# Optimization experiments

Measured on AMD Instinct MI355X. Metric: run time of the kernel, lower is better.

## Reference

```python
import math
import jax, jax.numpy as jnp
import numpy as np

NEG_INF = -jnp.inf


def setup_inputs() -> dict:
    key = jax.random.key(0)
    k1, k2, k3 = jax.random.split(key, 3)
    B, T, D = 2, 2048, 1024
    x = jax.random.normal(k1, (B, T, D), dtype=jnp.float32)
    w_qkv = jax.random.normal(k2, (3 * D, D), dtype=jnp.float32) * (1.0 / math.sqrt(D))
    w_out = jax.random.normal(k3, (D, D), dtype=jnp.float32) * (1.0 / math.sqrt(D))
    return {"x": x, "w_qkv": w_qkv, "w_out": w_out, "n_heads": 16, "k": 8}


def reference(x, w_qkv, w_out, n_heads, k):
    B, T, D = x.shape
    head_dim = D // n_heads
    scale = math.sqrt(head_dim)

    qkv = x @ w_qkv.T                                   # (B,T,3D), torch Linear: x W^T
    q, kk, v = jnp.split(qkv, 3, axis=-1)

    def split_heads(t):
        return t.reshape(B, T, n_heads, head_dim).transpose(0, 2, 1, 3)  # (B,H,T,dh)

    q, kk, v = split_heads(q), split_heads(kk), split_heads(v)

    scores = jnp.einsum("bhqd,bhkd->bhqk", q, kk) / scale  # (B,H,T,T)
    causal = jnp.tril(jnp.ones((T, T), dtype=bool))
    scores = jnp.where(causal, scores, NEG_INF)

    # per-row effective k: min(k, n_valid) with n_valid = row index + 1
    top_vals = jax.lax.top_k(scores, k)[0]                 # (B,H,T,k), sorted desc
    k_eff_idx = jnp.minimum(jnp.arange(1, T + 1), k) - 1   # (T,)
    thresh = jnp.take_along_axis(
        top_vals, k_eff_idx[None, None, :, None], axis=-1  # (B,H,T,1)
    )
    keep = scores >= thresh                                # ties kept, matching torch >=
    scores = jnp.where(keep, scores, NEG_INF)

    attn = jax.nn.softmax(scores, axis=-1)
    attn = jnp.nan_to_num(attn)                            # defensive; rows never all -inf
    out = jnp.einsum("bhqk,bhkd->bhqd", attn, v)
    out = out.transpose(0, 2, 1, 3).reshape(B, T, D)       # merge heads
    return out @ w_out.T
```

## Files before the change

### kernel.cpp

```cpp
#include <hip/hip_runtime.h>
#include <hip/hip_bf16.h>
#include <math.h>
#include <float.h>

#define NUM_B 2
#define SEQ_T 2048
#define DIM_D 1024
#define NH 16
#define DH 64
#define KDIM 1024
#define KSEL 8

#define CAP 32
#define MFMA_MARGIN 0.06f

typedef __attribute__((ext_vector_type(8))) short bf16x8v;
typedef __attribute__((ext_vector_type(4))) float f32x4v;
typedef __attribute__((ext_vector_type(4))) double f64x4v;

__device__ __forceinline__ float bf2f(unsigned int u) {
  union { unsigned int i; float f; } v; v.i = u << 16; return v.f;
}

__device__ __forceinline__ short f2bs(float f) {
  __hip_bfloat16 h = __float2bfloat16(f);
  return *(short*)&h;
}

__device__ __forceinline__ void split8(float4 x0, float4 x1,
                                       unsigned short* __restrict__ hp,
                                       unsigned short* __restrict__ lp) {
  unsigned short h[8], l[8];
  const float xs[8] = {x0.x, x0.y, x0.z, x0.w, x1.x, x1.y, x1.z, x1.w};
#pragma unroll
  for (int j = 0; j < 8; ++j) {
    const short hb = f2bs(xs[j]);
    h[j] = (unsigned short)hb;
    const float hf = bf2f((unsigned int)(unsigned short)hb);
    l[j] = (unsigned short)f2bs(xs[j] - hf);
  }
  *(uint4*)hp = *(const uint4*)h;
  *(uint4*)lp = *(const uint4*)l;
}

__device__ __forceinline__ void split4(float4 x,
                                       unsigned short* __restrict__ hp,
                                       unsigned short* __restrict__ lp) {
  unsigned short h[4], l[4];
  const float xs[4] = {x.x, x.y, x.z, x.w};
#pragma unroll
  for (int j = 0; j < 4; ++j) {
    const short hb = f2bs(xs[j]);
    h[j] = (unsigned short)hb;
    const float hf = bf2f((unsigned int)(unsigned short)hb);
    l[j] = (unsigned short)f2bs(xs[j] - hf);
  }
  *(uint2*)hp = *(const uint2*)h;
  *(uint2*)lp = *(const uint2*)l;
}

__global__ __launch_bounds__(512) void gemm_qk(
    const float* __restrict__ A, const float* __restrict__ Bm,
    float* __restrict__ qbuf, float* __restrict__ kbuf,
    unsigned short* __restrict__ kbf) {
  __shared__ __align__(16) float As[64][36];
  __shared__ __align__(16) float Bs[128][36];
  const int tid = threadIdx.x;
  const int lane = tid & 63;
  const int w = tid >> 6;
  const int row0 = blockIdx.y * 64;
  const int col0 = blockIdx.x * 128;
  const int lrA = tid >> 3;
  const int lkA = (tid & 7) << 2;
  const int lrB = tid >> 2;
  const int lkB = (tid & 3) << 3;
  const float* ap = A + (size_t)(row0 + lrA) * KDIM + lkA;
  const float* bp = Bm + (size_t)(col0 + lrB) * KDIM + lkB;
  const int wr = (w >> 2) << 5;
  const int wc = (w & 3) << 5;
  const int li = lane & 15;
  const int lk4 = lane >> 4;

  int rowof[4], colof[4];
  {
    f64x4v pr = {0.0, 0.0, 0.0, 0.0};
    f64x4v pc = {0.0, 0.0, 0.0, 0.0};
    const double vidx = (double)li;
    pr = __builtin_amdgcn_mfma_f64_16x16x4f64(vidx, 1.0, pr, 0, 0, 0);
    pc = __builtin_amdgcn_mfma_f64_16x16x4f64(1.0, vidx, pc, 0, 0, 0);
#pragma unroll
    for (int vj = 0; vj < 4; ++vj) {
      rowof[vj] = (int)(pr[vj] * 0.25 + 0.5);
      colof[vj] = (int)(pc[vj] * 0.25 + 0.5);
    }
  }

  f64x4v acc[2][2];
#pragma unroll
  for (int m = 0; m < 2; ++m)
#pragma unroll
    for (int n = 0; n < 2; ++n)
      acc[m][n] = (f64x4v){0.0, 0.0, 0.0, 0.0};

  float4 ra = *(const float4*)(ap);
  float4 rb0 = *(const float4*)(bp);
  float4 rb1 = *(const float4*)(bp + 4);
  for (int k0 = 0; k0 < KDIM; k0 += 32) {
    __syncthreads();
    *(float4*)&As[lrA][lkA] = ra;
    *(float4*)&Bs[lrB][lkB] = rb0;
    *(float4*)&Bs[lrB][lkB + 4] = rb1;
    if (k0 + 32 < KDIM) {
      ra = *(const float4*)(ap + k0 + 32);
      rb0 = *(const float4*)(bp + k0 + 32);
      rb1 = *(const float4*)(bp + k0 + 36);
    }
    __syncthreads();
#pragma unroll
    for (int ks = 0; ks < 32; ks += 4) {
      const int kk = ks + lk4;
      const double af0 = (double)As[wr + li][kk];
      const double af1 = (double)As[wr + 16 + li][kk];
      const double bf0 = (double)Bs[wc + li][kk];
      const double bf1 = (double)Bs[wc + 16 + li][kk];
      acc[0][0] = __builtin_amdgcn_mfma_f64_16x16x4f64(af0, bf0, acc[0][0], 0, 0, 0);
      acc[0][1] = __builtin_amdgcn_mfma_f64_16x16x4f64(af0, bf1, acc[0][1], 0, 0, 0);
      acc[1][0] = __builtin_amdgcn_mfma_f64_16x16x4f64(af1, bf0, acc[1][0], 0, 0, 0);
      acc[1][1] = __builtin_amdgcn_mfma_f64_16x16x4f64(af1, bf1, acc[1][1], 0, 0, 0);
    }
  }

  const int bb = row0 >> 11;
  const int t0 = row0 & 2047;
#pragma unroll
  for (int m = 0; m < 2; ++m)
#pragma unroll
    for (int n = 0; n < 2; ++n)
#pragma unroll
      for (int vj = 0; vj < 4; ++vj) {
        const int r = wr + 16 * m + rowof[vj];
        const int gc = col0 + wc + 16 * n + colof[vj];
        const int qi = gc >> 10;
        const int head = (gc & 1023) >> 6;
        const int d = gc & 63;
        const int t = t0 + r;
        const float fv = (float)acc[m][n][vj];
        float* dst = ((qi == 0) ? qbuf : kbuf) +
                     (size_t)(bb * NH + head) * SEQ_T * DH;
        dst[(size_t)t * DH + d] = fv;
        if (qi == 1) {
          unsigned short* kb = kbf + ((size_t)(bb * NH + head) << 17);
          const int key = t & 127;
          const int off =
              (((t >> 7) << 13) | (key << 6) | d) ^ ((key & 7) << 3);
          __hip_bfloat16 hb = __float2bfloat16(fv);
          kb[off] = *(unsigned short*)&hb;
        }
      }
}

__global__ __launch_bounds__(512) void gemm_v(
    const float* __restrict__ A, const float* __restrict__ Bm,
    unsigned short* __restrict__ vbuf) {
  __shared__ __align__(16) unsigned short Ah[64][40];
  __shared__ __align__(16) unsigned short Al[64][40];
  __shared__ __align__(16) unsigned short Bh[128][40];
  __shared__ __align__(16) unsigned short Bl[128][40];
  const int tid = threadIdx.x;
  const int lane = tid & 63;
  const int w = tid >> 6;
  const int row0 = blockIdx.y * 64;
  const int col0v = blockIdx.x * 128;
  const int lrA = tid >> 3;
  const int lkA = (tid & 7) << 2;
  const int lrB = tid >> 2;
  const int lkB = (tid & 3) << 3;
  const float* ap = A + (size_t)(row0 + lrA) * KDIM + lkA;
  const float* bp = Bm + (size_t)(col0v + lrB) * KDIM + lkB;
  const int wr = (w >> 2) << 5;
  const int wc = (w & 3) << 5;
  const int li = lane & 15;
  const int kA = (lane >> 4) << 3;

  f32x4v acc[2][2];
#pragma unroll
  for (int m = 0; m < 2; ++m)
#pragma unroll
    for (int n = 0; n < 2; ++n)
      acc[m][n] = (f32x4v){0.f, 0.f, 0.f, 0.f};

  float4 ra = *(const float4*)(ap);
  float4 rb0 = *(const float4*)(bp);
  float4 rb1 = *(const float4*)(bp + 4);
  for (int k0 = 0; k0 < KDIM; k0 += 32) {
    __syncthreads();
    split4(ra, &Ah[lrA][lkA], &Al[lrA][lkA]);
    split8(rb0, rb1, &Bh[lrB][lkB], &Bl[lrB][lkB]);
    if (k0 + 32 < KDIM) {
      ra = *(const float4*)(ap + k0 + 32);
      rb0 = *(const float4*)(bp + k0 + 32);
      rb1 = *(const float4*)(bp + k0 + 36);
    }
    __syncthreads();
    bf16x8v ah[2], al[2], bh[2], bl[2];
#pragma unroll
    for (int m = 0; m < 2; ++m) {
      ah[m] = *(const bf16x8v*)&Ah[wr + 16 * m + li][kA];
      al[m] = *(const bf16x8v*)&Al[wr + 16 * m + li][kA];
      bh[m] = *(const bf16x8v*)&Bh[wc + 16 * m + li][kA];
      bl[m] = *(const bf16x8v*)&Bl[wc + 16 * m + li][kA];
    }
#pragma unroll
    for (int m = 0; m < 2; ++m)
#pragma unroll
      for (int n = 0; n < 2; ++n) {
        acc[m][n] = __builtin_amdgcn_mfma_f32_16x16x32_bf16(ah[m], bh[n], acc[m][n], 0, 0, 0);
        acc[m][n] = __builtin_amdgcn_mfma_f32_16x16x32_bf16(ah[m], bl[n], acc[m][n], 0, 0, 0);
        acc[m][n] = __builtin_amdgcn_mfma_f32_16x16x32_bf16(al[m], bh[n], acc[m][n], 0, 0, 0);
      }
  }

  const int bb = row0 >> 11;
  const int t0 = row0 & 2047;
  const int r4 = (lane >> 4) << 2;
#pragma unroll
  for (int m = 0; m < 2; ++m)
#pragma unroll
    for (int n = 0; n < 2; ++n)
#pragma unroll
      for (int j = 0; j < 4; ++j) {
        const int t = t0 + wr + 16 * m + r4 + j;
        const int vcol = col0v + wc + 16 * n + li;
        const int head = vcol >> 6;
        const int d = vcol & 63;
        vbuf[(size_t)(bb * NH + head) * SEQ_T * DH + (size_t)t * DH + d] =
            (unsigned short)f2bs(acc[m][n][j]);
      }
}

__global__ __launch_bounds__(512) void attn_topk(
    const float* __restrict__ q, const float* __restrict__ kmat,
    const unsigned short* __restrict__ kbf,
    const unsigned short* __restrict__ v, unsigned short* __restrict__ ctx) {
  __shared__ __align__(16) unsigned short kt[128 * 64];
  __shared__ double cs64[128][CAP];
  __shared__ short ckey[128][CAP];
  __shared__ int ccnt[128];
  __shared__ double rthr[128];
  __shared__ float rmx[128];

  const int tid = threadIdx.x;
  const int lane = tid & 63;
  const int w = tid >> 6;
  const int bh = blockIdx.x & 31;
  const int u = blockIdx.x >> 5;
  const int g = (u < 8) ? u : 23 - u;
  const int t0 = g << 7;
  const size_t kbase = (size_t)bh * SEQ_T * DH;
  const int wrow0 = t0 + (w << 4);
  const int kA = (lane >> 4) << 3;
  const int rbase = wrow0 + ((lane >> 4) << 2);

  bf16x8v qa0, qa1;
  {
    const float* qr = q + kbase + (size_t)(wrow0 + (lane & 15)) * DH;
    const float4 x0 = *(const float4*)(qr + kA);
    const float4 x1 = *(const float4*)(qr + kA + 4);
    const float4 y0 = *(const float4*)(qr + 32 + kA);
    const float4 y1 = *(const float4*)(qr + 32 + kA + 4);
    qa0[0] = f2bs(x0.x); qa0[1] = f2bs(x0.y);
    qa0[2] = f2bs(x0.z); qa0[3] = f2bs(x0.w);
    qa0[4] = f2bs(x1.x); qa0[5] = f2bs(x1.y);
    qa0[6] = f2bs(x1.z); qa0[7] = f2bs(x1.w);
    qa1[0] = f2bs(y0.x); qa1[1] = f2bs(y0.y);
    qa1[2] = f2bs(y0.z); qa1[3] = f2bs(y0.w);
    qa1[4] = f2bs(y1.x); qa1[5] = f2bs(y1.y);
    qa1[6] = f2bs(y1.z); qa1[7] = f2bs(y1.w);
  }

  const uint4* ksrc = (const uint4*)(kbf + ((size_t)bh << 17));
  const int nt = (t0 >> 7) + 1;
  const int wmax = wrow0 + 15;

  float tq[4][8];
#pragma unroll
  for (int j = 0; j < 4; ++j)
#pragma unroll
    for (int m = 0; m < 8; ++m) tq[j][m] = -FLT_MAX;

  for (int T = 0; T < nt; ++T) {
    if (T) __syncthreads();
    {
      const uint4* st = ksrc + (size_t)T * 1024;
      uint4* dv = (uint4*)kt;
#pragma unroll
      for (int i = 0; i < 2; ++i) dv[i * 512 + tid] = st[i * 512 + tid];
    }
    __syncthreads();
    const int glim0 = (wmax - (T << 7)) >> 4;
    const int glim = glim0 > 7 ? 7 : glim0;
    for (int gt = 0; gt <= glim; ++gt) {
      const int kk = (gt << 4) + (lane & 15);
      const int key = (T << 7) + kk;
      const int b0 = ((kk << 7) | (kA << 1)) ^ ((kk & 7) << 4);
      const int b1 = ((kk << 7) | ((32 + kA) << 1)) ^ ((kk & 7) << 4);
      const bf16x8v kb0 = *(const bf16x8v*)((const char*)kt + b0);
      const bf16x8v kb1 = *(const bf16x8v*)((const char*)kt + b1);
      f32x4v acc = {0.f, 0.f, 0.f, 0.f};
      acc = __builtin_amdgcn_mfma_f32_16x16x32_bf16(qa0, kb0, acc, 0, 0, 0);
      acc = __builtin_amdgcn_mfma_f32_16x16x32_bf16(qa1, kb1, acc, 0, 0, 0);
#pragma unroll
      for (int j = 0; j < 4; ++j) {
        float sc = acc[j] * 0.125f;
        sc = (key <= rbase + j) ? sc : -FLT_MAX;
        if (sc > tq[j][7]) {
          float s = sc;
#pragma unroll
          for (int m = 0; m < 8; ++m) {
            const float hi = fmaxf(tq[j][m], s);
            s = fminf(tq[j][m], s);
            tq[j][m] = hi;
          }
        }
      }
    }
  }

#pragma unroll
  for (int j = 0; j < 4; ++j) {
#pragma unroll
    for (int xm = 1; xm < 16; xm <<= 1) {
      float m[8];
#pragma unroll
      for (int i = 0; i < 8; ++i) {
        const float pb = __shfl_xor(tq[j][7 - i], xm);
        m[i] = fmaxf(tq[j][i], pb);
      }
#pragma unroll
      for (int d = 4; d >= 1; d >>= 1)
#pragma unroll
        for (int i = 0; i < 8; ++i)
          if ((i & d) == 0 && (i | d) < 8) {
            const float hi = fmaxf(m[i], m[i | d]);
            const float lo = fminf(m[i], m[i | d]);
            m[i] = hi;
            m[i | d] = lo;
          }
#pragma unroll
      for (int i = 0; i < 8; ++i) tq[j][i] = m[i];
    }
  }
  float thrj[4];
#pragma unroll
  for (int j = 0; j < 4; ++j) {
    const int kf = (rbase + j + 1 < KSEL) ? (rbase + j + 1) : KSEL;
    float th = tq[j][7];
#pragma unroll
    for (int m = 0; m < 8; ++m)
      if (m == kf - 1) th = tq[j][m];
    thrj[j] = th - MFMA_MARGIN;
  }

  if (tid < 128) ccnt[tid] = 0;
  __syncthreads();

  for (int T = 0; T < nt; ++T) {
    if (T) __syncthreads();
    {
      const uint4* st = ksrc + (size_t)T * 1024;
      uint4* dv = (uint4*)kt;
#pragma unroll
      for (int i = 0; i < 2; ++i) dv[i * 512 + tid] = st[i * 512 + tid];
    }
    __syncthreads();
    const int glim0 = (wmax - (T << 7)) >> 4;
    const int glim = glim0 > 7 ? 7 : glim0;
    for (int gt = 0; gt <= glim; ++gt) {
      const int kk = (gt << 4) + (lane & 15);
      const int key = (T << 7) + kk;
      const int b0 = ((kk << 7) | (kA << 1)) ^ ((kk & 7) << 4);
      const int b1 = ((kk << 7) | ((32 + kA) << 1)) ^ ((kk & 7) << 4);
      const bf16x8v kb0 = *(const bf16x8v*)((const char*)kt + b0);
      const bf16x8v kb1 = *(const bf16x8v*)((const char*)kt + b1);
      f32x4v acc = {0.f, 0.f, 0.f, 0.f};
      acc = __builtin_amdgcn_mfma_f32_16x16x32_bf16(qa0, kb0, acc, 0, 0, 0);
      acc = __builtin_amdgcn_mfma_f32_16x16x32_bf16(qa1, kb1, acc, 0, 0, 0);
#pragma unroll
      for (int j = 0; j < 4; ++j) {
        const float sc = acc[j] * 0.125f;
        if (key <= rbase + j && sc >= thrj[j]) {
          const int rl = (w << 4) + ((lane >> 4) << 2) + j;
          const int p = atomicAdd(&ccnt[rl], 1);
          if (p < CAP) ckey[rl][p] = (short)key;
        }
      }
    }
  }

  const int lid = lane & 31;
  for (int rp = 0; rp < 8; ++rp) {
    const int rl = (w << 4) + (rp << 1) + (lane >> 5);
    const int ncc = ccnt[rl] < CAP ? ccnt[rl] : CAP;
    if (lid < ncc) {
      const int key = ckey[rl][lid];
      const float* qr = q + kbase + (size_t)(t0 + rl) * DH;
      const float* kr = kmat + kbase + (size_t)key * DH;
      double s = 0.0;
#pragma unroll
      for (int d4 = 0; d4 < 16; ++d4) {
        const float4 qq = *(const float4*)(qr + (d4 << 2));
        const float4 kq = *(const float4*)(kr + (d4 << 2));
        s = fma((double)qq.x, (double)kq.x, s);
        s = fma((double)qq.y, (double)kq.y, s);
        s = fma((double)qq.z, (double)kq.z, s);
        s = fma((double)qq.w, (double)kq.w, s);
      }
      cs64[rl][lid] = s * 0.125;
    }
  }
  __syncthreads();

  if (lane < 16) {
    const int rl = (w << 4) + lane;
    const int trow = t0 + rl;
    const int ncc = ccnt[rl] < CAP ? ccnt[rl] : CAP;
    double a64[8];
#pragma unroll
    for (int j = 0; j < 8; ++j) a64[j] = -DBL_MAX;
    for (int l = 0; l < ncc; ++l) {
      double sv = cs64[rl][l];
#pragma unroll
      for (int j = 0; j < 8; ++j) {
        const double hi = fmax(a64[j], sv);
        sv = fmin(a64[j], sv);
        a64[j] = hi;
      }
    }
    const int kf = (trow + 1 < KSEL) ? (trow + 1) : KSEL;
    double th = a64[7];
#pragma unroll
    for (int j = 0; j < 8; ++j)
      if (j == kf - 1) th = a64[j];
    rthr[rl] = th;
    rmx[rl] = (float)a64[0];
  }
  __syncthreads();

  for (int rg = 0; rg < 4; ++rg) {
    const int rlb = (w << 4) + (rg << 2);
    float acv[4] = {0.f, 0.f, 0.f, 0.f};
    float Zs[4] = {0.f, 0.f, 0.f, 0.f};
    int ncs[4];
    double ths[4];
    float mxs[4];
#pragma unroll
    for (int j = 0; j < 4; ++j) {
      const int rl = rlb + j;
      ncs[j] = ccnt[rl] < CAP ? ccnt[rl] : CAP;
      ths[j] = rthr[rl];
      mxs[j] = rmx[rl];
    }
    int nmax = ncs[0];
#pragma unroll
    for (int j = 1; j < 4; ++j) nmax = ncs[j] > nmax ? ncs[j] : nmax;
    for (int l = 0; l < nmax; ++l) {
#pragma unroll
      for (int j = 0; j < 4; ++j) {
        const int rl = rlb + j;
        if (l < ncs[j]) {
          const double s = cs64[rl][l];
          const float wgl = (s >= ths[j]) ? expf((float)s - mxs[j]) : 0.f;
          Zs[j] += wgl;
          acv[j] = fmaf(
              wgl,
              bf2f((unsigned int)v[kbase + (size_t)ckey[rl][l] * DH + lane]),
              acv[j]);
        }
      }
    }
#pragma unroll
    for (int j = 0; j < 4; ++j) {
      const int trow = t0 + rlb + j;
      __hip_bfloat16 h = __float2bfloat16(acv[j] / Zs[j]);
      ctx[((size_t)(bh >> 4) * SEQ_T + trow) * DIM_D + (bh & 15) * DH + lane] =
          *(unsigned short*)&h;
    }
  }
}

__global__ __launch_bounds__(512) void gemm_out(
    const unsigned short* __restrict__ A, const float* __restrict__ Bm,
    float* __restrict__ obuf) {
  __shared__ __align__(16) unsigned short Ah[64][40];
  __shared__ __align__(16) unsigned short Bh[128][40];
  __shared__ __align__(16) unsigned short Bl[128][40];
  const int tid = threadIdx.x;
  const int lane = tid & 63;
  const int w = tid >> 6;
  const int row0 = blockIdx.y * 64;
  const int col0 = blockIdx.x * 128;
  const int lrA = tid >> 3;
  const int lkA = (tid & 7) << 2;
  const int lrB = tid >> 2;
  const int lkB = (tid & 3) << 3;
  const unsigned short* ap = A + (size_t)(row0 + lrA) * KDIM + lkA;
  const float* bp = Bm + (size_t)(col0 + lrB) * KDIM + lkB;
  const int wr = (w >> 2) << 5;
  const int wc = (w & 3) << 5;
  const int li = lane & 15;
  const int kA = (lane >> 4) << 3;

  f32x4v acc[2][2];
#pragma unroll
  for (int m = 0; m < 2; ++m)
#pragma unroll
    for (int n = 0; n < 2; ++n)
      acc[m][n] = (f32x4v){0.f, 0.f, 0.f, 0.f};

  uint2 ua = *(const uint2*)(ap);
  float4 rb0 = *(const float4*)(bp);
  float4 rb1 = *(const float4*)(bp + 4);
  for (int k0 = 0; k0 < KDIM; k0 += 32) {
    __syncthreads();
    *(uint2*)&Ah[lrA][lkA] = ua;
    split8(rb0, rb1, &Bh[lrB][lkB], &Bl[lrB][lkB]);
    if (k0 + 32 < KDIM) {
      ua = *(const uint2*)(ap + k0 + 32);
      rb0 = *(const float4*)(bp + k0 + 32);
      rb1 = *(const float4*)(bp + k0 + 36);
    }
    __syncthreads();
    bf16x8v ah[2], bh[2], bl[2];
#pragma unroll
    for (int m = 0; m < 2; ++m) {
      ah[m] = *(const bf16x8v*)&Ah[wr + 16 * m + li][kA];
      bh[m] = *(const bf16x8v*)&Bh[wc + 16 * m + li][kA];
      bl[m] = *(const bf16x8v*)&Bl[wc + 16 * m + li][kA];
    }
#pragma unroll
    for (int m = 0; m < 2; ++m)
#pragma unroll
      for (int n = 0; n < 2; ++n) {
        acc[m][n] = __builtin_amdgcn_mfma_f32_16x16x32_bf16(ah[m], bh[n], acc[m][n], 0, 0, 0);
        acc[m][n] = __builtin_amdgcn_mfma_f32_16x16x32_bf16(ah[m], bl[n], acc[m][n], 0, 0, 0);
      }
  }

  const int r4 = (lane >> 4) << 2;
#pragma unroll
  for (int m = 0; m < 2; ++m)
#pragma unroll
    for (int n = 0; n < 2; ++n)
#pragma unroll
      for (int j = 0; j < 4; ++j) {
        const int r = row0 + wr + 16 * m + r4 + j;
        const int c = col0 + wc + 16 * n + li;
        obuf[(size_t)r * DIM_D + c] = acc[m][n][j];
      }
}

extern "C" void kernel_launch(void* const* d_in, const int* in_sizes, int n_in,
                              void* d_out, int out_size, void* d_ws,
                              size_t ws_size, hipStream_t stream) {
  (void)out_size; (void)ws_size;
  const float* x = (const float*)d_in[0];
  const float* wqkv = (const float*)d_in[1];
  const float* wout = (const float*)d_in[2];
  for (int i = 0; i < n_in; ++i) {
    if (in_sizes[i] == NUM_B * SEQ_T * DIM_D) x = (const float*)d_in[i];
    else if (in_sizes[i] == 3 * DIM_D * DIM_D) wqkv = (const float*)d_in[i];
    else if (in_sizes[i] == DIM_D * DIM_D) wout = (const float*)d_in[i];
  }
  float* out = (float*)d_out;

  const size_t qkv_elems = (size_t)NUM_B * NH * SEQ_T * DH;
  float* qbuf = (float*)d_ws;
  float* kbuf = qbuf + qkv_elems;
  unsigned short* vbuf = (unsigned short*)(kbuf + qkv_elems);
  unsigned short* ctxb = vbuf + qkv_elems;
  unsigned short* kbf = ctxb + (size_t)NUM_B * SEQ_T * DIM_D;

  gemm_qk<<<dim3(2 * DIM_D / 128, NUM_B * SEQ_T / 64), 512, 0, stream>>>(
      x, wqkv, qbuf, kbuf, kbf);
  gemm_v<<<dim3(DIM_D / 128, NUM_B * SEQ_T / 64), 512, 0, stream>>>(
      x, wqkv + (size_t)2 * DIM_D * KDIM, vbuf);
  attn_topk<<<dim3(NUM_B * NH * (SEQ_T / 128)), 512, 0, stream>>>(
      qbuf, kbuf, kbf, vbuf, ctxb);
  gemm_out<<<dim3(DIM_D / 128, NUM_B * SEQ_T / 64), 512, 0, stream>>>(
      ctxb, wout, out);
}
```

Baseline: 596.6 us.

## Track key indices in per-lane top-k and drop second scoring pass

Each lane's running top-8 buffer now stores the key index next to each bf16 MFMA score. Candidates above the margin-adjusted threshold are emitted straight from these local buffers, so the second full sweep over K is removed. That sweep reloaded K tiles into shared memory and recomputed the MFMA scores. In exchange, the insertion network carries an extra integer array with select-based swaps, which adds register pressure. In near-tie cases a candidate that falls outside a single lane's local top-8 could be missed.

```diff
diff --git a/kernel.cpp b/kernel.cpp
--- a/kernel.cpp
+++ b/kernel.cpp
@@ -283,10 +283,11 @@
   const int wmax = wrow0 + 15;
 
   float tq[4][8];
+  int tk[4][8];
 #pragma unroll
   for (int j = 0; j < 4; ++j)
 #pragma unroll
-    for (int m = 0; m < 8; ++m) tq[j][m] = -FLT_MAX;
+    for (int m = 0; m < 8; ++m) { tq[j][m] = -FLT_MAX; tk[j][m] = 0; }
 
   for (int T = 0; T < nt; ++T) {
     if (T) __syncthreads();
@@ -315,17 +316,29 @@
         sc = (key <= rbase + j) ? sc : -FLT_MAX;
         if (sc > tq[j][7]) {
           float s = sc;
+          int kx = key;
 #pragma unroll
           for (int m = 0; m < 8; ++m) {
-            const float hi = fmaxf(tq[j][m], s);
-            s = fminf(tq[j][m], s);
-            tq[j][m] = hi;
+            const bool c = s > tq[j][m];
+            const float vh = c ? s : tq[j][m];
+            const float vl = c ? tq[j][m] : s;
+            const int kh = c ? kx : tk[j][m];
+            const int kl = c ? tk[j][m] : kx;
+            tq[j][m] = vh;
+            tk[j][m] = kh;
+            s = vl;
+            kx = kl;
           }
         }
       }
     }
   }
 
+  float tm[4][8];
+#pragma unroll
+  for (int j = 0; j < 4; ++j)
+#pragma unroll
+    for (int m = 0; m < 8; ++m) tm[j][m] = tq[j][m];
 #pragma unroll
   for (int j = 0; j < 4; ++j) {
 #pragma unroll
@@ -333,8 +346,8 @@
       float m[8];
 #pragma unroll
       for (int i = 0; i < 8; ++i) {
-        const float pb = __shfl_xor(tq[j][7 - i], xm);
-        m[i] = fmaxf(tq[j][i], pb);
+        const float pb = __shfl_xor(tm[j][7 - i], xm);
+        m[i] = fmaxf(tm[j][i], pb);
       }
 #pragma unroll
       for (int d = 4; d >= 1; d >>= 1)
@@ -347,55 +360,35 @@
             m[i | d] = lo;
           }
 #pragma unroll
-      for (int i = 0; i < 8; ++i) tq[j][i] = m[i];
+      for (int i = 0; i < 8; ++i) tm[j][i] = m[i];
     }
   }
   float thrj[4];
 #pragma unroll
   for (int j = 0; j < 4; ++j) {
     const int kf = (rbase + j + 1 < KSEL) ? (rbase + j + 1) : KSEL;
-    float th = tq[j][7];
+    float th = tm[j][7];
 #pragma unroll
     for (int m = 0; m < 8; ++m)
-      if (m == kf - 1) th = tq[j][m];
+      if (m == kf - 1) th = tm[j][m];
     thrj[j] = th - MFMA_MARGIN;
   }
 
   if (tid < 128) ccnt[tid] = 0;
   __syncthreads();
 
-  for (int T = 0; T < nt; ++T) {
-    if (T) __syncthreads();
-    {
-      const uint4* st = ksrc + (size_t)T * 1024;
-      uint4* dv = (uint4*)kt;
-#pragma unroll
-      for (int i = 0; i < 2; ++i) dv[i * 512 + tid] = st[i * 512 + tid];
-    }
-    __syncthreads();
-    const int glim0 = (wmax - (T << 7)) >> 4;
-    const int glim = glim0 > 7 ? 7 : glim0;
-    for (int gt = 0; gt <= glim; ++gt) {
-      const int kk = (gt << 4) + (lane & 15);
-      const int key = (T << 7) + kk;
-      const int b0 = ((kk << 7) | (kA << 1)) ^ ((kk & 7) << 4);
-      const int b1 = ((kk << 7) | ((32 + kA) << 1)) ^ ((kk & 7) << 4);
-      const bf16x8v kb0 = *(const bf16x8v*)((const char*)kt + b0);
-      const bf16x8v kb1 = *(const bf16x8v*)((const char*)kt + b1);
-      f32x4v acc = {0.f, 0.f, 0.f, 0.f};
-      acc = __builtin_amdgcn_mfma_f32_16x16x32_bf16(qa0, kb0, acc, 0, 0, 0);
-      acc = __builtin_amdgcn_mfma_f32_16x16x32_bf16(qa1, kb1, acc, 0, 0, 0);
-#pragma unroll
-      for (int j = 0; j < 4; ++j) {
-        const float sc = acc[j] * 0.125f;
-        if (key <= rbase + j && sc >= thrj[j]) {
-          const int rl = (w << 4) + ((lane >> 4) << 2) + j;
-          const int p = atomicAdd(&ccnt[rl], 1);
-          if (p < CAP) ckey[rl][p] = (short)key;
-        }
-      }
-    }
-  }
+#pragma unroll
+  for (int j = 0; j < 4; ++j) {
+    const int rl = (w << 4) + ((lane >> 4) << 2) + j;
+#pragma unroll
+    for (int m = 0; m < 8; ++m) {
+      if (tq[j][m] >= thrj[j]) {
+        const int p = atomicAdd(&ccnt[rl], 1);
+        if (p < CAP) ckey[rl][p] = (short)tk[j][m];
+      }
+    }
+  }
+  __syncthreads();
 
   const int lid = lane & 31;
   for (int rp = 0; rp < 8; ++rp) {
```

Measured after the change: 640.8 us. +7.4%, slower.
